# Kernel tuning notes

Hardware: AMD Instinct MI355X
Metric: run time of the kernel (lower is better)

The kernel has to match this reference:

```python
import jax, jax.numpy as jnp
import numpy as np

EPS = 1e-5
NEG_SLOPE = 0.2


def _batched_dynamic_conv(x, kernels):
    # x: [B, C, H, W]; kernels: [B, Cout, Cin, 3, 3]. Per-sample distinct
    # kernels == one grouped conv with feature_group_count = B.
    B, C, H, W = x.shape
    Cout = kernels.shape[1]
    xg = x.reshape(1, B * C, H, W)
    kg = kernels.reshape(B * Cout, C, 3, 3)
    y = jax.lax.conv_general_dilated(
        xg, kg, window_strides=(1, 1), padding=((1, 1), (1, 1)),
        feature_group_count=B,
        dimension_numbers=('NCHW', 'OIHW', 'NCHW'))
    return y.reshape(B, Cout, H, W)


def _instance_norm(y):
    # InstanceNorm2d(affine=False): per (b, c) over spatial dims, biased var.
    mean = jnp.mean(y, axis=(2, 3), keepdims=True)
    var = jnp.var(y, axis=(2, 3), keepdims=True)
    return (y - mean) * jax.lax.rsqrt(var + EPS)


def _leaky_relu(y):
    return jnp.where(y >= 0, y, NEG_SLOPE * y)


def setup_inputs() -> dict:
    key = jax.random.key(0)
    k1, k2, k3 = jax.random.split(key, 3)
    B, C, H, W = 16, 64, 128, 128
    x = jax.random.normal(k1, (B, C, H, W), dtype=jnp.float32)
    kernel1 = jax.random.normal(k2, (B, C, C, 3, 3), dtype=jnp.float32) * 0.05
    kernel2 = jax.random.normal(k3, (B, C, C, 3, 3), dtype=jnp.float32) * 0.05
    return {"x": x, "kernel1": kernel1, "kernel2": kernel2}


def reference(x, kernel1, kernel2):
    h = _leaky_relu(_instance_norm(_batched_dynamic_conv(x, kernel1)))
    h = _instance_norm(_batched_dynamic_conv(h, kernel2))
    return _leaky_relu(x + h)
```

## Files before the change

### kernel.cpp

```cpp
#include <hip/hip_runtime.h>
#include <stdint.h>
#include <stddef.h>

#define BATCH 16
#define CH    64
#define IH    128
#define IW    128
#define HW    (IH*IW)

#define PROW 8320
#define PB   1081600

typedef __attribute__((ext_vector_type(8))) short short8;
typedef __attribute__((ext_vector_type(4))) short short4v;
typedef __attribute__((ext_vector_type(4))) float f32x4;
typedef __attribute__((ext_vector_type(2))) float f32x2;

__device__ __forceinline__ float bf2f(short s) {
    union { unsigned int u; float f; } v;
    v.u = ((unsigned int)(unsigned short)s) << 16;
    return v.f;
}
__device__ __forceinline__ short f2bf(float f) {
    union { float f; unsigned int u; } v; v.f = f;
    unsigned int r = v.u + 0x7fffu + ((v.u >> 16) & 1u);
    return (short)(r >> 16);
}

__global__ __launch_bounds__(256) void pad_zero(short* __restrict__ xpad,
                                                short* __restrict__ hpad) {
    int bid = blockIdx.x;
    short* p = ((bid & 1) ? hpad : xpad) + (size_t)(bid >> 1) * PB;
    const short8 z = {0,0,0,0,0,0,0,0};
    #pragma unroll
    for (int i = 0; i < 17; ++i) {
        int s = i * 256 + threadIdx.x;
        if (s >= 4128) break;
        if (s < 2080) {
            int row = (s < 1040) ? 0 : 129;
            int o = (s < 1040 ? s : s - 1040) * 8;
            *(short8*)&p[(size_t)row * PROW + o] = z;
        } else {
            int u = s - 2080;
            int k = u & 3, col = (u >> 2) & 1, cc = (u >> 3) & 1, pr = (u >> 4) + 1;
            *(short8*)&p[(size_t)pr * PROW + cc * 4160 + (col ? 129 * 32 : 0) + k * 8] = z;
        }
    }
}

__global__ __launch_bounds__(256) void prep_x(const float* __restrict__ x,
                                              short* __restrict__ xpad) {
    __shared__ float tile[CH * 129];
    const int b = blockIdx.x >> 7;
    const int y = blockIdx.x & 127;
    const int t = threadIdx.x;
    const float* src = x + (size_t)b * CH * HW + (size_t)y * IW;
    #pragma unroll
    for (int i = 0; i < 32; ++i) {
        int lin = i * 256 + t;
        int c = lin >> 7, xx = lin & 127;
        tile[c * 129 + xx] = src[(size_t)c * HW + xx];
    }
    __syncthreads();
    unsigned int* dst = (unsigned int*)(xpad) + (size_t)b * (PB / 2) + (size_t)(y + 1) * (PROW / 2);
    #pragma unroll
    for (int j = 0; j < 16; ++j) {
        int lin = j * 256 + t;
        int c2 = lin & 31, xx = lin >> 5;
        unsigned int lo = (unsigned int)(unsigned short)f2bf(tile[(2 * c2) * 129 + xx]);
        unsigned int hi = (unsigned int)(unsigned short)f2bf(tile[(2 * c2 + 1) * 129 + xx]);
        dst[(c2 >> 4) * 2080 + (xx + 1) * 16 + (c2 & 15)] = lo | (hi << 16);
    }
}

__global__ __launch_bounds__(256) void prep_w(const float* __restrict__ w1,
                                              const float* __restrict__ w2,
                                              short* __restrict__ w1t,
                                              short* __restrict__ w2t) {
    int bid = blockIdx.x;
    const float* src = w1; short* dst = w1t;
    if (bid >= 256) { src = w2; dst = w2t; bid -= 256; }
    int gt = bid * 256 + threadIdx.x;
    int ci   = gt & 31;
    int cout = (gt >> 5) & 63;
    int cc   = (gt >> 11) & 1;
    int b    = gt >> 12;
    const float* s = src + ((size_t)(b * 64 + cout)) * 576 + (cc * 32 + ci) * 9;
    short* d = dst + ((size_t)(b * 2 + cc) * 9) * 2048 + cout * 32 + ci;
    #pragma unroll
    for (int tap = 0; tap < 9; ++tap)
        d[tap * 2048] = f2bf(s[tap]);
}

__global__ __launch_bounds__(256, 4) void conv_kernel(
    const short* __restrict__ in, const short* __restrict__ wt,
    short* __restrict__ out,
    float* __restrict__ part_s, float* __restrict__ part_q) {

    const int b    = blockIdx.y;
    const int t    = threadIdx.x;
    const int lane = t & 63;
    const int wave = t >> 6;
    const int l15  = lane & 15;
    const int q    = lane >> 4;
    const int ph   = wave & 1;
    const int wr   = wave >> 1;
    const int y0   = (blockIdx.x << 1) + wr;
    const int xb   = ph * 64;

    const short* wgl = wt + (size_t)b * 36864;
    const short* inB = in + (size_t)b * PB;
    const int aoff = l15 * 32 + q * 8;
    const int boff = (xb + l15) * 32 + q * 8;

    const f32x4 zero4 = {0.f, 0.f, 0.f, 0.f};
    f32x4 acc[4][4];
    #pragma unroll
    for (int mi = 0; mi < 4; ++mi)
        #pragma unroll
        for (int ni = 0; ni < 4; ++ni) acc[mi][ni] = zero4;

    #pragma unroll
    for (int cc = 0; cc < 2; ++cc) {
        #pragma unroll
        for (int tap = 0; tap < 9; ++tap) {
            const int dy = tap / 3, dx = tap % 3;
            const short* arow = wgl + (cc * 9 + tap) * 2048 + aoff;
            const short* brow = inB + (size_t)(y0 + dy) * PROW + cc * 4160 + dx * 32 + boff;
            short8 a[4], bb[4];
            #pragma unroll
            for (int mi = 0; mi < 4; ++mi)
                a[mi] = *(const short8*)&arow[mi * 512];
            #pragma unroll
            for (int ni = 0; ni < 4; ++ni)
                bb[ni] = *(const short8*)&brow[ni * 512];
            #pragma unroll
            for (int mi = 0; mi < 4; ++mi)
                #pragma unroll
                for (int ni = 0; ni < 4; ++ni)
                    acc[mi][ni] = __builtin_amdgcn_mfma_f32_16x16x32_bf16(
                        a[mi], bb[ni], acc[mi][ni], 0, 0, 0);
        }
    }

    const int pbase = ((b * 128 + y0) * 2 + ph) * 64;
    #pragma unroll
    for (int mi = 0; mi < 4; ++mi) {
        float psum[4] = {0.f,0.f,0.f,0.f};
        float psq[4]  = {0.f,0.f,0.f,0.f};
        #pragma unroll
        for (int ni = 0; ni < 4; ++ni) {
            int xx = xb + ni * 16 + l15;
            size_t base = (size_t)b * PB + (size_t)(1 + y0) * PROW
                          + (mi >> 1) * 4160 + (size_t)(1 + xx) * 32
                          + (mi & 1) * 16 + q * 4;
            short4v o;
            #pragma unroll
            for (int g = 0; g < 4; ++g) {
                float v = acc[mi][ni][g];
                o[g] = f2bf(v);
                psum[g] += v;
                psq[g]  += v * v;
            }
            *(short4v*)&out[base] = o;
        }
        #pragma unroll
        for (int g = 0; g < 4; ++g) {
            float s = psum[g], s2 = psq[g];
            #pragma unroll
            for (int off = 1; off < 16; off <<= 1) {
                s  += __shfl_xor(s,  off, 64);
                s2 += __shfl_xor(s2, off, 64);
            }
            if (l15 == 0) {
                int idx = pbase + mi * 16 + q * 4 + g;
                part_s[idx] = s;
                part_q[idx] = s2;
            }
        }
    }
}

__global__ __launch_bounds__(256) void finalize_stats(const float* __restrict__ part_s,
                                                      const float* __restrict__ part_q,
                                                      float* __restrict__ nrm) {
    int i = blockIdx.x * 256 + threadIdx.x;
    if (i >= BATCH * CH) return;
    int b = i >> 6, c = i & 63;
    float s = 0.f, s2 = 0.f;
    const float* ps = part_s + (size_t)b * 128 * 2 * 64 + c;
    const float* pq = part_q + (size_t)b * 128 * 2 * 64 + c;
    #pragma unroll 4
    for (int r = 0; r < 256; ++r) {
        s  += ps[r * 64];
        s2 += pq[r * 64];
    }
    const float inv = 1.0f / (float)HW;
    float mean = s * inv;
    float var = s2 * inv - mean * mean;
    float scale = rsqrtf(var + 1e-5f);
    f32x2 sb = {scale, -mean * scale};
    ((f32x2*)nrm)[i] = sb;
}

__global__ __launch_bounds__(256) void norm_leaky(short* __restrict__ hpad,
                                                  const float* __restrict__ nrm) {
    const int bid = blockIdx.x;
    const int b = bid >> 7, y = bid & 127;
    short* row = hpad + (size_t)b * PB + (size_t)(y + 1) * PROW;
    const int t = threadIdx.x;
    #pragma unroll
    for (int i = 0; i < 4; ++i) {
        int s = i * 256 + t;
        int c8 = s & 3, xx = (s >> 2) & 127, cc = s >> 9;
        short* p = row + cc * 4160 + (xx + 1) * 32 + c8 * 8;
        const f32x2* nb = (const f32x2*)nrm + b * CH + cc * 32 + c8 * 8;
        short8 v = *(const short8*)p;
        short8 o;
        #pragma unroll
        for (int j = 0; j < 8; ++j) {
            f32x2 sb = nb[j];
            float f = sb.x * bf2f(v[j]) + sb.y;
            f = f >= 0.f ? f : 0.2f * f;
            o[j] = f2bf(f);
        }
        *(short8*)p = o;
    }
}

__global__ __launch_bounds__(256) void final_kernel(const float* __restrict__ x,
                                                    const short* __restrict__ y2,
                                                    const float* __restrict__ nrm,
                                                    float* __restrict__ out) {
    __shared__ float tile[64 * 65];
    const int x0 = blockIdx.x * 64;
    const int y  = blockIdx.y;
    const int b  = blockIdx.z;
    const int t  = threadIdx.x;
    const f32x2* nb = (const f32x2*)nrm + b * CH;
    const size_t rowb = (size_t)b * PB + (size_t)(y + 1) * PROW;
    #pragma unroll
    for (int i = 0; i < 2; ++i) {
        int s = i * 256 + t;
        int xx = s >> 3;
        int c0 = (s & 7) * 8;
        int cc = c0 >> 5, cl = c0 & 31;
        short8 v = *(const short8*)&y2[rowb + cc * 4160 + (size_t)(x0 + xx + 1) * 32 + cl];
        #pragma unroll
        for (int j = 0; j < 8; ++j) {
            f32x2 sb = nb[c0 + j];
            tile[(c0 + j) * 65 + xx] = sb.x * bf2f(v[j]) + sb.y;
        }
    }
    __syncthreads();
    #pragma unroll
    for (int i = 0; i < 4; ++i) {
        int lin = i * 1024 + t * 4;
        int c = lin >> 6;
        int xx = lin & 63;
        size_t g = ((size_t)(b * CH + c) * IH + y) * IW + x0 + xx;
        f32x4 xv = *(const f32x4*)&x[g];
        f32x4 o;
        #pragma unroll
        for (int k = 0; k < 4; ++k) {
            float f = xv[k] + tile[c * 65 + xx + k];
            o[k] = f >= 0.f ? f : 0.2f * f;
        }
        *(f32x4*)&out[g] = o;
    }
}

extern "C" void kernel_launch(void* const* d_in, const int* in_sizes, int n_in,
                              void* d_out, int out_size, void* d_ws, size_t ws_size,
                              hipStream_t stream) {
    const float* x  = (const float*)d_in[0];
    const float* w1 = (const float*)d_in[1];
    const float* w2 = (const float*)d_in[2];
    float* out = (float*)d_out;
    char* ws = (char*)d_ws;

    const size_t SZ_PAD  = 34611200ull;
    const size_t SZ_PART = 1048576ull;
    short* xpad = (short*)(ws);
    short* hpad = (short*)(ws + SZ_PAD);
    short* w1t  = (short*)(ws + 2 * SZ_PAD);
    short* w2t  = (short*)(ws + 2 * SZ_PAD + 1179648ull);
    float* ps1  = (float*)(ws + 2 * SZ_PAD + 2359296ull);
    float* pq1  = (float*)(ws + 2 * SZ_PAD + 2359296ull + SZ_PART);
    float* ps2  = (float*)(ws + 2 * SZ_PAD + 2359296ull + 2 * SZ_PART);
    float* pq2  = (float*)(ws + 2 * SZ_PAD + 2359296ull + 3 * SZ_PART);
    float* nrm1 = (float*)(ws + 2 * SZ_PAD + 2359296ull + 4 * SZ_PART);
    float* nrm2 = nrm1 + BATCH * CH * 2;

    if (ws_size < 2 * SZ_PAD + 2359296ull + 4 * SZ_PART + 8192) return;

    pad_zero<<<32, 256, 0, stream>>>(xpad, hpad);
    prep_x<<<BATCH * IH, 256, 0, stream>>>(x, xpad);
    prep_w<<<512, 256, 0, stream>>>(w1, w2, w1t, w2t);
    conv_kernel<<<dim3(64, 16), 256, 0, stream>>>(xpad, w1t, hpad, ps1, pq1);
    finalize_stats<<<4, 256, 0, stream>>>(ps1, pq1, nrm1);
    norm_leaky<<<2048, 256, 0, stream>>>(hpad, nrm1);
    conv_kernel<<<dim3(64, 16), 256, 0, stream>>>(hpad, w2t, xpad, ps2, pq2);
    finalize_stats<<<4, 256, 0, stream>>>(ps2, pq2, nrm2);
    final_kernel<<<dim3(2, 128, 16), 256, 0, stream>>>(x, xpad, nrm2, out);
}
```

Measured before the change: 287.1 us.

## Stage conv input rows in LDS, merge prep kernels, parallelize stats finalize

The three prep kernels (padding zeroing, x conversion, weight transpose) are merged into one launch to cut launch overhead. The conv kernel now copies the four padded input rows it needs into shared memory with global_load_lds and reads the B operands from LDS rather than from global memory. This is meant to avoid repeated global reads across the 9 taps and the two waves sharing a row. Launch bounds drop from 4 to 2 blocks per CU because of the roughly 66 KB LDS tile, which cuts occupancy. finalize_stats now uses one block per batch with a shared-memory reduction instead of four sparse blocks.

New measurement: 239.2 us. -16.7%, faster.

```diff
diff --git a/kernel.cpp b/kernel.cpp
--- a/kernel.cpp
+++ b/kernel.cpp
@@ -27,75 +27,83 @@
     return (short)(r >> 16);
 }
 
-__global__ __launch_bounds__(256) void pad_zero(short* __restrict__ xpad,
-                                                short* __restrict__ hpad) {
-    int bid = blockIdx.x;
-    short* p = ((bid & 1) ? hpad : xpad) + (size_t)(bid >> 1) * PB;
-    const short8 z = {0,0,0,0,0,0,0,0};
-    #pragma unroll
-    for (int i = 0; i < 17; ++i) {
-        int s = i * 256 + threadIdx.x;
-        if (s >= 4128) break;
-        if (s < 2080) {
-            int row = (s < 1040) ? 0 : 129;
-            int o = (s < 1040 ? s : s - 1040) * 8;
-            *(short8*)&p[(size_t)row * PROW + o] = z;
-        } else {
-            int u = s - 2080;
-            int k = u & 3, col = (u >> 2) & 1, cc = (u >> 3) & 1, pr = (u >> 4) + 1;
-            *(short8*)&p[(size_t)pr * PROW + cc * 4160 + (col ? 129 * 32 : 0) + k * 8] = z;
-        }
-    }
-}
-
-__global__ __launch_bounds__(256) void prep_x(const float* __restrict__ x,
-                                              short* __restrict__ xpad) {
-    __shared__ float tile[CH * 129];
-    const int b = blockIdx.x >> 7;
-    const int y = blockIdx.x & 127;
+__device__ __forceinline__ void gload_lds16(const short* g, short* l) {
+    __builtin_amdgcn_global_load_lds(
+        (const __attribute__((address_space(1))) void*)g,
+        (__attribute__((address_space(3))) void*)l, 16, 0, 0);
+}
+
+__global__ __launch_bounds__(256) void prep_all(const float* __restrict__ x,
+                                                const float* __restrict__ w1,
+                                                const float* __restrict__ w2,
+                                                short* __restrict__ xpad,
+                                                short* __restrict__ hpad,
+                                                short* __restrict__ w1t,
+                                                short* __restrict__ w2t) {
+    const int bid = blockIdx.x;
     const int t = threadIdx.x;
-    const float* src = x + (size_t)b * CH * HW + (size_t)y * IW;
-    #pragma unroll
-    for (int i = 0; i < 32; ++i) {
-        int lin = i * 256 + t;
-        int c = lin >> 7, xx = lin & 127;
-        tile[c * 129 + xx] = src[(size_t)c * HW + xx];
-    }
-    __syncthreads();
-    unsigned int* dst = (unsigned int*)(xpad) + (size_t)b * (PB / 2) + (size_t)(y + 1) * (PROW / 2);
-    #pragma unroll
-    for (int j = 0; j < 16; ++j) {
-        int lin = j * 256 + t;
-        int c2 = lin & 31, xx = lin >> 5;
-        unsigned int lo = (unsigned int)(unsigned short)f2bf(tile[(2 * c2) * 129 + xx]);
-        unsigned int hi = (unsigned int)(unsigned short)f2bf(tile[(2 * c2 + 1) * 129 + xx]);
-        dst[(c2 >> 4) * 2080 + (xx + 1) * 16 + (c2 & 15)] = lo | (hi << 16);
-    }
-}
-
-__global__ __launch_bounds__(256) void prep_w(const float* __restrict__ w1,
-                                              const float* __restrict__ w2,
-                                              short* __restrict__ w1t,
-                                              short* __restrict__ w2t) {
-    int bid = blockIdx.x;
-    const float* src = w1; short* dst = w1t;
-    if (bid >= 256) { src = w2; dst = w2t; bid -= 256; }
-    int gt = bid * 256 + threadIdx.x;
-    int ci   = gt & 31;
-    int cout = (gt >> 5) & 63;
-    int cc   = (gt >> 11) & 1;
-    int b    = gt >> 12;
-    const float* s = src + ((size_t)(b * 64 + cout)) * 576 + (cc * 32 + ci) * 9;
-    short* d = dst + ((size_t)(b * 2 + cc) * 9) * 2048 + cout * 32 + ci;
-    #pragma unroll
-    for (int tap = 0; tap < 9; ++tap)
-        d[tap * 2048] = f2bf(s[tap]);
-}
-
-__global__ __launch_bounds__(256, 4) void conv_kernel(
+    if (bid < 2048) {
+        __shared__ float tile[CH * 129];
+        const int b = bid >> 7;
+        const int y = bid & 127;
+        const float* src = x + (size_t)b * CH * HW + (size_t)y * IW;
+        #pragma unroll
+        for (int i = 0; i < 32; ++i) {
+            int lin = i * 256 + t;
+            int c = lin >> 7, xx = lin & 127;
+            tile[c * 129 + xx] = src[(size_t)c * HW + xx];
+        }
+        __syncthreads();
+        unsigned int* dst = (unsigned int*)(xpad) + (size_t)b * (PB / 2) + (size_t)(y + 1) * (PROW / 2);
+        #pragma unroll
+        for (int j = 0; j < 16; ++j) {
+            int lin = j * 256 + t;
+            int c2 = lin & 31, xx = lin >> 5;
+            unsigned int lo = (unsigned int)(unsigned short)f2bf(tile[(2 * c2) * 129 + xx]);
+            unsigned int hi = (unsigned int)(unsigned short)f2bf(tile[(2 * c2 + 1) * 129 + xx]);
+            dst[(c2 >> 4) * 2080 + (xx + 1) * 16 + (c2 & 15)] = lo | (hi << 16);
+        }
+    } else if (bid < 2560) {
+        int b2 = bid - 2048;
+        const float* src = w1; short* dst = w1t;
+        if (b2 >= 256) { src = w2; dst = w2t; b2 -= 256; }
+        int gt = b2 * 256 + t;
+        int ci   = gt & 31;
+        int cout = (gt >> 5) & 63;
+        int cc   = (gt >> 11) & 1;
+        int b    = gt >> 12;
+        const float* s = src + ((size_t)(b * 64 + cout)) * 576 + (cc * 32 + ci) * 9;
+        short* d = dst + ((size_t)(b * 2 + cc) * 9) * 2048 + cout * 32 + ci;
+        #pragma unroll
+        for (int tap = 0; tap < 9; ++tap)
+            d[tap * 2048] = f2bf(s[tap]);
+    } else {
+        int b2 = bid - 2560;
+        short* p = ((b2 & 1) ? hpad : xpad) + (size_t)(b2 >> 1) * PB;
+        const short8 z = {0,0,0,0,0,0,0,0};
+        #pragma unroll
+        for (int i = 0; i < 17; ++i) {
+            int s = i * 256 + t;
+            if (s >= 4128) break;
+            if (s < 2080) {
+                int row = (s < 1040) ? 0 : 129;
+                int o = (s < 1040 ? s : s - 1040) * 8;
+                *(short8*)&p[(size_t)row * PROW + o] = z;
+            } else {
+                int u = s - 2080;
+                int k = u & 3, col = (u >> 2) & 1, cc = (u >> 3) & 1, pr = (u >> 4) + 1;
+                *(short8*)&p[(size_t)pr * PROW + cc * 4160 + (col ? 129 * 32 : 0) + k * 8] = z;
+            }
+        }
+    }
+}
+
+__global__ __launch_bounds__(256, 2) void conv_kernel(
     const short* __restrict__ in, const short* __restrict__ wt,
     short* __restrict__ out,
     float* __restrict__ part_s, float* __restrict__ part_q) {
+
+    __shared__ short act[4 * PROW];
 
     const int b    = blockIdx.y;
     const int t    = threadIdx.x;
@@ -108,8 +116,20 @@
     const int y0   = (blockIdx.x << 1) + wr;
     const int xb   = ph * 64;
 
+    const short* inB = in + (size_t)b * PB;
+
+    {
+        const short* grow = inB + (size_t)((blockIdx.x << 1) + wave) * PROW;
+        short* lrow = &act[wave * PROW];
+        #pragma unroll
+        for (int i = 0; i < 16; ++i)
+            gload_lds16(grow + i * 512 + lane * 8, lrow + i * 512);
+        if (lane < 16)
+            gload_lds16(grow + 16 * 512 + lane * 8, lrow + 16 * 512);
+    }
+    __syncthreads();
+
     const short* wgl = wt + (size_t)b * 36864;
-    const short* inB = in + (size_t)b * PB;
     const int aoff = l15 * 32 + q * 8;
     const int boff = (xb + l15) * 32 + q * 8;
 
@@ -126,14 +146,14 @@
         for (int tap = 0; tap < 9; ++tap) {
             const int dy = tap / 3, dx = tap % 3;
             const short* arow = wgl + (cc * 9 + tap) * 2048 + aoff;
-            const short* brow = inB + (size_t)(y0 + dy) * PROW + cc * 4160 + dx * 32 + boff;
+            const int bbase = (wr + dy) * PROW + cc * 4160 + dx * 32 + boff;
             short8 a[4], bb[4];
             #pragma unroll
             for (int mi = 0; mi < 4; ++mi)
                 a[mi] = *(const short8*)&arow[mi * 512];
             #pragma unroll
             for (int ni = 0; ni < 4; ++ni)
-                bb[ni] = *(const short8*)&brow[ni * 512];
+                bb[ni] = *(const short8*)&act[bbase + ni * 512];
             #pragma unroll
             for (int mi = 0; mi < 4; ++mi)
                 #pragma unroll
@@ -184,23 +204,31 @@
 __global__ __launch_bounds__(256) void finalize_stats(const float* __restrict__ part_s,
                                                       const float* __restrict__ part_q,
                                                       float* __restrict__ nrm) {
-    int i = blockIdx.x * 256 + threadIdx.x;
-    if (i >= BATCH * CH) return;
-    int b = i >> 6, c = i & 63;
+    __shared__ float red[2][4][64];
+    const int b = blockIdx.x;
+    const int c = threadIdx.x & 63;
+    const int g = threadIdx.x >> 6;
+    const float* ps = part_s + (size_t)b * 16384 + c;
+    const float* pq = part_q + (size_t)b * 16384 + c;
     float s = 0.f, s2 = 0.f;
-    const float* ps = part_s + (size_t)b * 128 * 2 * 64 + c;
-    const float* pq = part_q + (size_t)b * 128 * 2 * 64 + c;
-    #pragma unroll 4
-    for (int r = 0; r < 256; ++r) {
-        s  += ps[r * 64];
-        s2 += pq[r * 64];
-    }
-    const float inv = 1.0f / (float)HW;
-    float mean = s * inv;
-    float var = s2 * inv - mean * mean;
-    float scale = rsqrtf(var + 1e-5f);
-    f32x2 sb = {scale, -mean * scale};
-    ((f32x2*)nrm)[i] = sb;
+    #pragma unroll 8
+    for (int r = 0; r < 64; ++r) {
+        s  += ps[(g * 64 + r) * 64];
+        s2 += pq[(g * 64 + r) * 64];
+    }
+    red[0][g][c] = s;
+    red[1][g][c] = s2;
+    __syncthreads();
+    if (threadIdx.x < 64) {
+        float S = red[0][0][c] + red[0][1][c] + red[0][2][c] + red[0][3][c];
+        float Q = red[1][0][c] + red[1][1][c] + red[1][2][c] + red[1][3][c];
+        const float inv = 1.0f / (float)HW;
+        float mean = S * inv;
+        float var = Q * inv - mean * mean;
+        float scale = rsqrtf(var + 1e-5f);
+        f32x2 sb = {scale, -mean * scale};
+        ((f32x2*)nrm)[b * CH + c] = sb;
+    }
 }
 
 __global__ __launch_bounds__(256) void norm_leaky(short* __restrict__ hpad,
@@ -294,13 +322,11 @@
 
     if (ws_size < 2 * SZ_PAD + 2359296ull + 4 * SZ_PART + 8192) return;
 
-    pad_zero<<<32, 256, 0, stream>>>(xpad, hpad);
-    prep_x<<<BATCH * IH, 256, 0, stream>>>(x, xpad);
-    prep_w<<<512, 256, 0, stream>>>(w1, w2, w1t, w2t);
+    prep_all<<<2592, 256, 0, stream>>>(x, w1, w2, xpad, hpad, w1t, w2t);
     conv_kernel<<<dim3(64, 16), 256, 0, stream>>>(xpad, w1t, hpad, ps1, pq1);
-    finalize_stats<<<4, 256, 0, stream>>>(ps1, pq1, nrm1);
+    finalize_stats<<<16, 256, 0, stream>>>(ps1, pq1, nrm1);
     norm_leaky<<<2048, 256, 0, stream>>>(hpad, nrm1);
     conv_kernel<<<dim3(64, 16), 256, 0, stream>>>(hpad, w2t, xpad, ps2, pq2);
-    finalize_stats<<<4, 256, 0, stream>>>(ps2, pq2, nrm2);
+    finalize_stats<<<16, 256, 0, stream>>>(ps2, pq2, nrm2);
     final_kernel<<<dim3(2, 128, 16), 256, 0, stream>>>(x, xpad, nrm2, out);
 }
```
